# Performance work log

Measured on AMD Instinct MI355X. Metric: run time of the kernel, lower is better.

## Reference

```python
import jax, jax.numpy as jnp
import numpy as np

N_NODES = 50000
N_EDGES = 800000
EMB = 96
HID = 2 * EMB


def setup_inputs() -> dict:
    key = jax.random.key(0)
    ks = jax.random.split(key, 8)
    h = jax.random.normal(ks[0], (N_NODES, EMB), dtype=jnp.float32)
    edge_attr = jax.random.normal(ks[1], (N_EDGES, EMB), dtype=jnp.float32)
    src = jax.random.randint(ks[2], (N_EDGES,), 0, N_NODES, dtype=jnp.int32)
    dst = jax.random.randint(ks[3], (N_EDGES,), 0, N_NODES, dtype=jnp.int32)
    W1 = jax.random.normal(ks[4], (EMB, HID), dtype=jnp.float32) * (1.0 / np.sqrt(EMB))
    b1 = jnp.zeros((HID,), dtype=jnp.float32)
    W2 = jax.random.normal(ks[5], (HID, EMB), dtype=jnp.float32) * (1.0 / np.sqrt(HID))
    b2 = jnp.zeros((EMB,), dtype=jnp.float32)
    eps = jnp.zeros((1,), dtype=jnp.float32)
    return {"h": h, "edge_attr": edge_attr, "src": src, "dst": dst,
            "W1": W1, "b1": b1, "W2": W2, "b2": b2, "eps": eps}


def reference(h, edge_attr, src, dst, W1, b1, W2, b2, eps):
    # message: m_e = h[src_e] + edge_attr_e   -> [E, EMB]
    m = h[src] + edge_attr
    # reduce: sum messages per destination node -> [N, EMB]
    aggr = jax.ops.segment_sum(m, dst, num_segments=N_NODES)
    # 2-layer MLP: Linear(EMB, 2*EMB) -> ReLU -> Linear(2*EMB, EMB)
    hidden = jax.nn.relu(aggr @ W1 + b1)
    mlp_out = hidden @ W2 + b2
    # GIN update: (1 + eps) * h + MLP(aggr)
    out = (1.0 + eps[0]) * h + mlp_out
    return out
```

## Files before the change

### kernel.cpp

```cpp
#include <hip/hip_runtime.h>

#define N_NODES 50000
#define N_EDGES 800000
#define EMB 96
#define HID 192

#define HIST_BLOCKS ((N_EDGES + 255) / 256)
#define CONV_BLOCKS ((2 * EMB * HID + 255) / 256)

typedef __attribute__((ext_vector_type(8))) short short8;
typedef __attribute__((ext_vector_type(4))) float f32x4;
typedef __attribute__((ext_vector_type(4))) unsigned short ushort4v;

static __device__ __forceinline__ unsigned short f2bf(float f) {
    union { float f; unsigned int u; } v; v.f = f;
    unsigned int u = v.u;
    return (unsigned short)((u + 0x7FFFu + ((u >> 16) & 1u)) >> 16);
}

__global__ __launch_bounds__(256) void hist_conv_kernel(
    const int* __restrict__ dst, int* __restrict__ counts,
    const float* __restrict__ W1, const float* __restrict__ W2,
    unsigned short* __restrict__ W1t, unsigned short* __restrict__ W2t)
{
    int b = blockIdx.x;
    if (b < HIST_BLOCKS) {
        int e = b * 256 + threadIdx.x;
        if (e < N_EDGES) atomicAdd(&counts[dst[e]], 1);
    } else {
        int i = (b - HIST_BLOCKS) * 256 + threadIdx.x;
        if (i < EMB * HID) {
            int n = i / EMB, k = i % EMB;
            W1t[i] = f2bf(W1[(size_t)k * HID + n]);
        } else if (i < 2 * EMB * HID) {
            int j = i - EMB * HID;
            int n = j / HID, k = j % HID;
            W2t[j] = f2bf(W2[(size_t)k * EMB + n]);
        }
    }
}

__global__ __launch_bounds__(1024) void scan_kernel(
    const int* __restrict__ counts, int* __restrict__ offsets)
{
    __shared__ int wave_sums[16];
    int t = threadIdx.x;
    int lane = t & 63, wave = t >> 6;
    int running = 0;
    int v_next = (t < N_NODES) ? counts[t] : 0;
    for (int base = 0; base < N_NODES; base += 1024) {
        int v = v_next;
        int nidx = base + 1024 + t;
        v_next = (nidx < N_NODES) ? counts[nidx] : 0;
        int x = v;
        #pragma unroll
        for (int d = 1; d < 64; d <<= 1) {
            int y = __shfl_up(x, d);
            if (lane >= d) x += y;
        }
        if (lane == 63) wave_sums[wave] = x;
        __syncthreads();
        if (t < 16) {
            int s = wave_sums[t];
            #pragma unroll
            for (int d = 1; d < 16; d <<= 1) {
                int y = __shfl_up(s, d);
                if (t >= d) s += y;
            }
            wave_sums[t] = s;
        }
        __syncthreads();
        int woff = wave ? wave_sums[wave - 1] : 0;
        if (base + t < N_NODES) offsets[base + t] = running + woff + x - v;
        int total = wave_sums[15];
        __syncthreads();
        running += total;
    }
    if (t == 0) offsets[N_NODES] = running;
}

__global__ __launch_bounds__(256) void fill_kernel(
    const int* __restrict__ src, const int* __restrict__ dst,
    const int* __restrict__ offsets, int* __restrict__ cursor,
    int2* __restrict__ pairs)
{
    int e = blockIdx.x * 256 + threadIdx.x;
    if (e < N_EDGES) {
        int d = dst[e];
        int pos = offsets[d] + atomicAdd(&cursor[d], 1);
        pairs[pos] = make_int2(e, src[e]);
    }
}

__global__ __launch_bounds__(192) void gather_kernel4(
    const f32x4* __restrict__ h4, const f32x4* __restrict__ ea4,
    const int* __restrict__ offsets, const int2* __restrict__ pairs,
    unsigned short* __restrict__ aggr_bf)
{
    int n = blockIdx.x * 8 + threadIdx.x / 24;
    int c = threadIdx.x % 24;
    if (n >= N_NODES) return;
    int beg = offsets[n], end = offsets[n + 1];
    f32x4 a0 = {0.f, 0.f, 0.f, 0.f}, a1 = a0, a2 = a0, a3 = a0;
    int i = beg;
    for (; i + 4 <= end; i += 4) {
        int2 q0 = pairs[i], q1 = pairs[i + 1], q2 = pairs[i + 2], q3 = pairs[i + 3];
        f32x4 e0 = __builtin_nontemporal_load(&ea4[(size_t)q0.x * 24 + c]);
        f32x4 e1 = __builtin_nontemporal_load(&ea4[(size_t)q1.x * 24 + c]);
        f32x4 e2 = __builtin_nontemporal_load(&ea4[(size_t)q2.x * 24 + c]);
        f32x4 e3 = __builtin_nontemporal_load(&ea4[(size_t)q3.x * 24 + c]);
        f32x4 g0 = h4[(size_t)q0.y * 24 + c];
        f32x4 g1 = h4[(size_t)q1.y * 24 + c];
        f32x4 g2 = h4[(size_t)q2.y * 24 + c];
        f32x4 g3 = h4[(size_t)q3.y * 24 + c];
        a0 += e0 + g0;
        a1 += e1 + g1;
        a2 += e2 + g2;
        a3 += e3 + g3;
    }
    for (; i < end; ++i) {
        int2 q = pairs[i];
        f32x4 e = __builtin_nontemporal_load(&ea4[(size_t)q.x * 24 + c]);
        f32x4 g = h4[(size_t)q.y * 24 + c];
        a0 += e + g;
    }
    f32x4 acc = (a0 + a1) + (a2 + a3);
    ushort4v o;
    o.x = f2bf(acc.x); o.y = f2bf(acc.y); o.z = f2bf(acc.z); o.w = f2bf(acc.w);
    *(ushort4v*)(aggr_bf + (size_t)n * EMB + c * 4) = o;
}

__global__ __launch_bounds__(256) void mlp_fused(
    const unsigned short* __restrict__ aggr_bf,
    const unsigned short* __restrict__ W1t, const float* __restrict__ b1,
    const unsigned short* __restrict__ W2t, const float* __restrict__ b2,
    const float* __restrict__ h, const float* __restrict__ eps,
    float* __restrict__ out)
{
    __shared__ unsigned short sW1[HID * 104];
    int t = threadIdx.x;
    const unsigned int* p1 = (const unsigned int*)W1t;
    for (int i = t; i < HID * (EMB / 2); i += 256) {
        int n = i / (EMB / 2), c2 = i % (EMB / 2);
        *(unsigned int*)&sW1[n * 104 + c2 * 2] = p1[(size_t)n * (EMB / 2) + c2];
    }
    __syncthreads();

    int wave = t >> 6, lane = t & 63;
    int m0 = (blockIdx.x * 4 + wave) * 16;
    bool active = (m0 < N_NODES);
    int quad = lane >> 4, col = lane & 15;
    int m = m0 + col;

    f32x4 acc1[12];
    #pragma unroll
    for (int c = 0; c < 12; ++c) acc1[c] = (f32x4){0.f, 0.f, 0.f, 0.f};
    if (active) {
        #pragma unroll
        for (int ks = 0; ks < 3; ++ks) {
            short8 af = *(const short8*)(aggr_bf + (size_t)m * EMB + ks * 32 + quad * 8);
            #pragma unroll
            for (int c = 0; c < 12; ++c) {
                short8 bf = *(const short8*)(sW1 + (c * 16 + col) * 104 + ks * 32 + quad * 8);
                acc1[c] = __builtin_amdgcn_mfma_f32_16x16x32_bf16(af, bf, acc1[c], 0, 0, 0);
            }
        }
    }
    __syncthreads();

    if (active) {
        unsigned short* sH = sW1 + wave * (16 * 200);
        #pragma unroll
        for (int c = 0; c < 12; ++c) {
            float bias = b1[c * 16 + col];
            #pragma unroll
            for (int r = 0; r < 4; ++r) {
                int lr = quad * 4 + r;
                sH[lr * 200 + c * 16 + col] = f2bf(fmaxf(acc1[c][r] + bias, 0.f));
            }
        }
        f32x4 acc2[6];
        #pragma unroll
        for (int c = 0; c < 6; ++c) acc2[c] = (f32x4){0.f, 0.f, 0.f, 0.f};
        #pragma unroll
        for (int ks = 0; ks < 6; ++ks) {
            short8 af = *(const short8*)(sH + col * 200 + ks * 32 + quad * 8);
            #pragma unroll
            for (int c = 0; c < 6; ++c) {
                short8 bf = *(const short8*)(W2t + (size_t)(c * 16 + col) * HID + ks * 32 + quad * 8);
                acc2[c] = __builtin_amdgcn_mfma_f32_16x16x32_bf16(af, bf, acc2[c], 0, 0, 0);
            }
        }
        float s = 1.f + eps[0];
        #pragma unroll
        for (int c = 0; c < 6; ++c) {
            float bias = b2[c * 16 + col];
            #pragma unroll
            for (int r = 0; r < 4; ++r) {
                int row = m0 + quad * 4 + r;
                size_t idx = (size_t)row * EMB + c * 16 + col;
                out[idx] = acc2[c][r] + bias + s * h[idx];
            }
        }
    }
}

extern "C" void kernel_launch(void* const* d_in, const int* in_sizes, int n_in,
                              void* d_out, int out_size, void* d_ws, size_t ws_size,
                              hipStream_t stream) {
    const float* h         = (const float*)d_in[0];
    const float* edge_attr = (const float*)d_in[1];
    const int*   src       = (const int*)d_in[2];
    const int*   dst       = (const int*)d_in[3];
    const float* W1        = (const float*)d_in[4];
    const float* b1        = (const float*)d_in[5];
    const float* W2        = (const float*)d_in[6];
    const float* b2        = (const float*)d_in[7];
    const float* eps       = (const float*)d_in[8];
    float* out = (float*)d_out;

    unsigned char* wsp = (unsigned char*)d_ws;
    unsigned short* aggr_bf = (unsigned short*)wsp; wsp += (size_t)N_NODES * EMB * 2;
    unsigned short* W1t     = (unsigned short*)wsp; wsp += (size_t)EMB * HID * 2;
    unsigned short* W2t     = (unsigned short*)wsp; wsp += (size_t)EMB * HID * 2;
    int2* pairs   = (int2*)wsp; wsp += (size_t)N_EDGES * sizeof(int2);
    int*  offsets = (int*)wsp;  wsp += (size_t)(N_NODES + 1) * sizeof(int);
    int*  counts  = (int*)wsp;  wsp += (size_t)N_NODES * sizeof(int);
    int*  cursor  = (int*)wsp;

    hipMemsetAsync(counts, 0, (size_t)2 * N_NODES * sizeof(int), stream);

    hist_conv_kernel<<<HIST_BLOCKS + CONV_BLOCKS, 256, 0, stream>>>(
        dst, counts, W1, W2, W1t, W2t);
    scan_kernel<<<1, 1024, 0, stream>>>(counts, offsets);
    fill_kernel<<<(N_EDGES + 255) / 256, 256, 0, stream>>>(src, dst, offsets, cursor, pairs);
    gather_kernel4<<<(N_NODES + 7) / 8, 192, 0, stream>>>(
        (const f32x4*)h, (const f32x4*)edge_attr, offsets, pairs, aggr_bf);
    mlp_fused<<<(N_NODES / 16 + 3) / 4, 256, 0, stream>>>(
        aggr_bf, W1t, b1, W2t, b2, h, eps, out);
}
```

Before: 596.7 us.

## Fuse all stages into one persistent kernel with software grid barriers

Replaces the five separate launches (histogram/convert, scan, fill, gather, MLP) with a single persistent kernel of 512 blocks that loops over work and synchronises stages with an atomic grid barrier. The single-block serial scan becomes a two-level parallel scan over per-block sums. This removes launch gaps and the serial scan, but relies on all 512 blocks being co-resident. It also cuts gather and MLP parallelism to a fixed grid, and the gather uses 32-thread groups with 8 of them idle.

```diff
diff --git a/kernel.cpp b/kernel.cpp
--- a/kernel.cpp
+++ b/kernel.cpp
@@ -5,8 +5,9 @@
 #define EMB 96
 #define HID 192
 
-#define HIST_BLOCKS ((N_EDGES + 255) / 256)
-#define CONV_BLOCKS ((2 * EMB * HID + 255) / 256)
+#define NB 512
+#define NT 256
+#define GSIZE (NB * NT)
 
 typedef __attribute__((ext_vector_type(8))) short short8;
 typedef __attribute__((ext_vector_type(4))) float f32x4;
@@ -18,188 +19,198 @@
     return (unsigned short)((u + 0x7FFFu + ((u >> 16) & 1u)) >> 16);
 }
 
-__global__ __launch_bounds__(256) void hist_conv_kernel(
-    const int* __restrict__ dst, int* __restrict__ counts,
-    const float* __restrict__ W1, const float* __restrict__ W2,
-    unsigned short* __restrict__ W1t, unsigned short* __restrict__ W2t)
+struct Params {
+    const float* h; const float* ea; const int* src; const int* dst;
+    const float* W1; const float* b1; const float* W2; const float* b2;
+    const float* eps; float* out;
+    unsigned short* aggr_bf; unsigned short* W1t; unsigned short* W2t;
+    int2* pairs; int* offsets; int* counts; int* cursor;
+    int* bar;
+    int* bsum; int* bpref;
+};
+
+static __device__ __forceinline__ void grid_barrier(int* arrive, int* gen) {
+    __syncthreads();
+    if (threadIdx.x == 0) {
+        int g = __hip_atomic_load(gen, __ATOMIC_RELAXED, __HIP_MEMORY_SCOPE_AGENT);
+        __threadfence();
+        int prev = __hip_atomic_fetch_add(arrive, 1, __ATOMIC_ACQ_REL,
+                                          __HIP_MEMORY_SCOPE_AGENT);
+        if (prev == NB - 1) {
+            __hip_atomic_store(arrive, 0, __ATOMIC_RELAXED, __HIP_MEMORY_SCOPE_AGENT);
+            __hip_atomic_fetch_add(gen, 1, __ATOMIC_RELEASE, __HIP_MEMORY_SCOPE_AGENT);
+        } else {
+            while (__hip_atomic_load(gen, __ATOMIC_ACQUIRE,
+                                     __HIP_MEMORY_SCOPE_AGENT) == g)
+                __builtin_amdgcn_s_sleep(1);
+        }
+    }
+    __syncthreads();
+    __threadfence();
+}
+
+__global__ __launch_bounds__(NT, 2) void mega_kernel(Params p)
 {
-    int b = blockIdx.x;
-    if (b < HIST_BLOCKS) {
-        int e = b * 256 + threadIdx.x;
-        if (e < N_EDGES) atomicAdd(&counts[dst[e]], 1);
-    } else {
-        int i = (b - HIST_BLOCKS) * 256 + threadIdx.x;
-        if (i < EMB * HID) {
-            int n = i / EMB, k = i % EMB;
-            W1t[i] = f2bf(W1[(size_t)k * HID + n]);
-        } else if (i < 2 * EMB * HID) {
-            int j = i - EMB * HID;
-            int n = j / HID, k = j % HID;
-            W2t[j] = f2bf(W2[(size_t)k * EMB + n]);
-        }
-    }
-}
-
-__global__ __launch_bounds__(1024) void scan_kernel(
-    const int* __restrict__ counts, int* __restrict__ offsets)
-{
-    __shared__ int wave_sums[16];
-    int t = threadIdx.x;
-    int lane = t & 63, wave = t >> 6;
-    int running = 0;
-    int v_next = (t < N_NODES) ? counts[t] : 0;
-    for (int base = 0; base < N_NODES; base += 1024) {
-        int v = v_next;
-        int nidx = base + 1024 + t;
-        v_next = (nidx < N_NODES) ? counts[nidx] : 0;
-        int x = v;
+    __shared__ __attribute__((aligned(16))) unsigned char smem[65536];
+    const int t = threadIdx.x, b = blockIdx.x;
+    const int gid = b * NT + t;
+    const int lane = t & 63, wave = t >> 6;
+
+    for (int e = gid; e < N_EDGES; e += GSIZE)
+        atomicAdd(&p.counts[p.dst[e]], 1);
+    for (int i = gid; i < EMB * HID; i += GSIZE) {
+        int n = i / EMB, k = i - n * EMB;
+        p.W1t[i] = f2bf(p.W1[(size_t)k * HID + n]);
+    }
+    for (int i = gid; i < EMB * HID; i += GSIZE) {
+        int n = i / HID, k = i - n * HID;
+        p.W2t[i] = f2bf(p.W2[(size_t)k * EMB + n]);
+    }
+    grid_barrier(&p.bar[0], &p.bar[1]);
+
+    int* ws4 = (int*)smem;
+    int v = (gid < N_NODES) ? p.counts[gid] : 0;
+    int x = v;
+    #pragma unroll
+    for (int d = 1; d < 64; d <<= 1) { int y = __shfl_up(x, d); if (lane >= d) x += y; }
+    if (lane == 63) ws4[wave] = x;
+    __syncthreads();
+    int s0 = ws4[0], s1 = ws4[1], s2 = ws4[2], s3 = ws4[3];
+    int wbase = (wave > 0 ? s0 : 0) + (wave > 1 ? s1 : 0) + (wave > 2 ? s2 : 0);
+    int locex = wbase + x - v;
+    if (t == 0) p.bsum[b] = s0 + s1 + s2 + s3;
+    grid_barrier(&p.bar[0], &p.bar[1]);
+
+    if (b == 0) {
+        int carry = 0;
         #pragma unroll
-        for (int d = 1; d < 64; d <<= 1) {
-            int y = __shfl_up(x, d);
-            if (lane >= d) x += y;
-        }
-        if (lane == 63) wave_sums[wave] = x;
+        for (int half = 0; half < NB / NT; ++half) {
+            int a = p.bsum[half * NT + t];
+            int xx = a;
+            #pragma unroll
+            for (int d = 1; d < 64; d <<= 1) { int y = __shfl_up(xx, d); if (lane >= d) xx += y; }
+            if (lane == 63) ws4[wave] = xx;
+            __syncthreads();
+            int q0 = ws4[0], q1 = ws4[1], q2 = ws4[2], q3 = ws4[3];
+            int wb = (wave > 0 ? q0 : 0) + (wave > 1 ? q1 : 0) + (wave > 2 ? q2 : 0);
+            p.bpref[half * NT + t] = carry + wb + xx - a;
+            __syncthreads();
+            carry += q0 + q1 + q2 + q3;
+        }
+    }
+    grid_barrier(&p.bar[0], &p.bar[1]);
+
+    if (gid < N_NODES) p.offsets[gid] = p.bpref[b] + locex;
+    if (gid == 0) p.offsets[N_NODES] = N_EDGES;
+    grid_barrier(&p.bar[0], &p.bar[1]);
+
+    for (int e = gid; e < N_EDGES; e += GSIZE) {
+        int d = p.dst[e];
+        int pos = p.offsets[d] + atomicAdd(&p.cursor[d], 1);
+        p.pairs[pos] = make_int2(e, p.src[e]);
+    }
+    grid_barrier(&p.bar[0], &p.bar[1]);
+
+    {
+        const f32x4* h4 = (const f32x4*)p.h;
+        const f32x4* ea4 = (const f32x4*)p.ea;
+        int g = t >> 5, c = t & 31;
+        for (int n = b * 8 + g; n < N_NODES; n += NB * 8) {
+            int beg = p.offsets[n], end = p.offsets[n + 1];
+            if (c < 24) {
+                f32x4 a0 = {0.f, 0.f, 0.f, 0.f}, a1 = a0, a2 = a0, a3 = a0;
+                int i = beg;
+                for (; i + 4 <= end; i += 4) {
+                    int2 q0 = p.pairs[i], q1 = p.pairs[i + 1];
+                    int2 q2 = p.pairs[i + 2], q3 = p.pairs[i + 3];
+                    f32x4 e0 = __builtin_nontemporal_load(&ea4[(size_t)q0.x * 24 + c]);
+                    f32x4 e1 = __builtin_nontemporal_load(&ea4[(size_t)q1.x * 24 + c]);
+                    f32x4 e2 = __builtin_nontemporal_load(&ea4[(size_t)q2.x * 24 + c]);
+                    f32x4 e3 = __builtin_nontemporal_load(&ea4[(size_t)q3.x * 24 + c]);
+                    f32x4 g0 = h4[(size_t)q0.y * 24 + c];
+                    f32x4 g1 = h4[(size_t)q1.y * 24 + c];
+                    f32x4 g2 = h4[(size_t)q2.y * 24 + c];
+                    f32x4 g3 = h4[(size_t)q3.y * 24 + c];
+                    a0 += e0 + g0;
+                    a1 += e1 + g1;
+                    a2 += e2 + g2;
+                    a3 += e3 + g3;
+                }
+                for (; i < end; ++i) {
+                    int2 q = p.pairs[i];
+                    f32x4 e = __builtin_nontemporal_load(&ea4[(size_t)q.x * 24 + c]);
+                    f32x4 gg = h4[(size_t)q.y * 24 + c];
+                    a0 += e + gg;
+                }
+                f32x4 acc = (a0 + a1) + (a2 + a3);
+                ushort4v o;
+                o.x = f2bf(acc.x); o.y = f2bf(acc.y);
+                o.z = f2bf(acc.z); o.w = f2bf(acc.w);
+                *(ushort4v*)(p.aggr_bf + (size_t)n * EMB + c * 4) = o;
+            }
+        }
+    }
+    grid_barrier(&p.bar[0], &p.bar[1]);
+
+    {
+        unsigned short* sW1 = (unsigned short*)smem;
+        unsigned short* sHid = (unsigned short*)(smem + HID * 104 * 2);
+        const unsigned int* p1 = (const unsigned int*)p.W1t;
+        for (int i = t; i < HID * (EMB / 2); i += NT) {
+            int n = i / (EMB / 2), c2 = i - n * (EMB / 2);
+            *(unsigned int*)&sW1[n * 104 + c2 * 2] = p1[n * (EMB / 2) + c2];
+        }
         __syncthreads();
-        if (t < 16) {
-            int s = wave_sums[t];
-            #pragma unroll
-            for (int d = 1; d < 16; d <<= 1) {
-                int y = __shfl_up(s, d);
-                if (t >= d) s += y;
-            }
-            wave_sums[t] = s;
-        }
-        __syncthreads();
-        int woff = wave ? wave_sums[wave - 1] : 0;
-        if (base + t < N_NODES) offsets[base + t] = running + woff + x - v;
-        int total = wave_sums[15];
-        __syncthreads();
-        running += total;
-    }
-    if (t == 0) offsets[N_NODES] = running;
-}
-
-__global__ __launch_bounds__(256) void fill_kernel(
-    const int* __restrict__ src, const int* __restrict__ dst,
-    const int* __restrict__ offsets, int* __restrict__ cursor,
-    int2* __restrict__ pairs)
-{
-    int e = blockIdx.x * 256 + threadIdx.x;
-    if (e < N_EDGES) {
-        int d = dst[e];
-        int pos = offsets[d] + atomicAdd(&cursor[d], 1);
-        pairs[pos] = make_int2(e, src[e]);
-    }
-}
-
-__global__ __launch_bounds__(192) void gather_kernel4(
-    const f32x4* __restrict__ h4, const f32x4* __restrict__ ea4,
-    const int* __restrict__ offsets, const int2* __restrict__ pairs,
-    unsigned short* __restrict__ aggr_bf)
-{
-    int n = blockIdx.x * 8 + threadIdx.x / 24;
-    int c = threadIdx.x % 24;
-    if (n >= N_NODES) return;
-    int beg = offsets[n], end = offsets[n + 1];
-    f32x4 a0 = {0.f, 0.f, 0.f, 0.f}, a1 = a0, a2 = a0, a3 = a0;
-    int i = beg;
-    for (; i + 4 <= end; i += 4) {
-        int2 q0 = pairs[i], q1 = pairs[i + 1], q2 = pairs[i + 2], q3 = pairs[i + 3];
-        f32x4 e0 = __builtin_nontemporal_load(&ea4[(size_t)q0.x * 24 + c]);
-        f32x4 e1 = __builtin_nontemporal_load(&ea4[(size_t)q1.x * 24 + c]);
-        f32x4 e2 = __builtin_nontemporal_load(&ea4[(size_t)q2.x * 24 + c]);
-        f32x4 e3 = __builtin_nontemporal_load(&ea4[(size_t)q3.x * 24 + c]);
-        f32x4 g0 = h4[(size_t)q0.y * 24 + c];
-        f32x4 g1 = h4[(size_t)q1.y * 24 + c];
-        f32x4 g2 = h4[(size_t)q2.y * 24 + c];
-        f32x4 g3 = h4[(size_t)q3.y * 24 + c];
-        a0 += e0 + g0;
-        a1 += e1 + g1;
-        a2 += e2 + g2;
-        a3 += e3 + g3;
-    }
-    for (; i < end; ++i) {
-        int2 q = pairs[i];
-        f32x4 e = __builtin_nontemporal_load(&ea4[(size_t)q.x * 24 + c]);
-        f32x4 g = h4[(size_t)q.y * 24 + c];
-        a0 += e + g;
-    }
-    f32x4 acc = (a0 + a1) + (a2 + a3);
-    ushort4v o;
-    o.x = f2bf(acc.x); o.y = f2bf(acc.y); o.z = f2bf(acc.z); o.w = f2bf(acc.w);
-    *(ushort4v*)(aggr_bf + (size_t)n * EMB + c * 4) = o;
-}
-
-__global__ __launch_bounds__(256) void mlp_fused(
-    const unsigned short* __restrict__ aggr_bf,
-    const unsigned short* __restrict__ W1t, const float* __restrict__ b1,
-    const unsigned short* __restrict__ W2t, const float* __restrict__ b2,
-    const float* __restrict__ h, const float* __restrict__ eps,
-    float* __restrict__ out)
-{
-    __shared__ unsigned short sW1[HID * 104];
-    int t = threadIdx.x;
-    const unsigned int* p1 = (const unsigned int*)W1t;
-    for (int i = t; i < HID * (EMB / 2); i += 256) {
-        int n = i / (EMB / 2), c2 = i % (EMB / 2);
-        *(unsigned int*)&sW1[n * 104 + c2 * 2] = p1[(size_t)n * (EMB / 2) + c2];
-    }
-    __syncthreads();
-
-    int wave = t >> 6, lane = t & 63;
-    int m0 = (blockIdx.x * 4 + wave) * 16;
-    bool active = (m0 < N_NODES);
-    int quad = lane >> 4, col = lane & 15;
-    int m = m0 + col;
-
-    f32x4 acc1[12];
-    #pragma unroll
-    for (int c = 0; c < 12; ++c) acc1[c] = (f32x4){0.f, 0.f, 0.f, 0.f};
-    if (active) {
-        #pragma unroll
-        for (int ks = 0; ks < 3; ++ks) {
-            short8 af = *(const short8*)(aggr_bf + (size_t)m * EMB + ks * 32 + quad * 8);
+        int quad = lane >> 4, col = lane & 15;
+        float s = 1.f + p.eps[0];
+        unsigned short* sH = sHid + wave * (16 * 200);
+        for (int rb = b; rb < (N_NODES + 63) / 64; rb += NB) {
+            int m0 = rb * 64 + wave * 16;
+            if (m0 >= N_NODES) continue;
+            int m = m0 + col;
+
+            f32x4 acc1[12];
+            #pragma unroll
+            for (int c = 0; c < 12; ++c) acc1[c] = (f32x4){0.f, 0.f, 0.f, 0.f};
+            #pragma unroll
+            for (int ks = 0; ks < 3; ++ks) {
+                short8 af = *(const short8*)(p.aggr_bf + (size_t)m * EMB + ks * 32 + quad * 8);
+                #pragma unroll
+                for (int c = 0; c < 12; ++c) {
+                    short8 bf = *(const short8*)(sW1 + (c * 16 + col) * 104 + ks * 32 + quad * 8);
+                    acc1[c] = __builtin_amdgcn_mfma_f32_16x16x32_bf16(af, bf, acc1[c], 0, 0, 0);
+                }
+            }
             #pragma unroll
             for (int c = 0; c < 12; ++c) {
-                short8 bf = *(const short8*)(sW1 + (c * 16 + col) * 104 + ks * 32 + quad * 8);
-                acc1[c] = __builtin_amdgcn_mfma_f32_16x16x32_bf16(af, bf, acc1[c], 0, 0, 0);
-            }
-        }
-    }
-    __syncthreads();
-
-    if (active) {
-        unsigned short* sH = sW1 + wave * (16 * 200);
-        #pragma unroll
-        for (int c = 0; c < 12; ++c) {
-            float bias = b1[c * 16 + col];
-            #pragma unroll
-            for (int r = 0; r < 4; ++r) {
-                int lr = quad * 4 + r;
-                sH[lr * 200 + c * 16 + col] = f2bf(fmaxf(acc1[c][r] + bias, 0.f));
-            }
-        }
-        f32x4 acc2[6];
-        #pragma unroll
-        for (int c = 0; c < 6; ++c) acc2[c] = (f32x4){0.f, 0.f, 0.f, 0.f};
-        #pragma unroll
-        for (int ks = 0; ks < 6; ++ks) {
-            short8 af = *(const short8*)(sH + col * 200 + ks * 32 + quad * 8);
+                float bias = p.b1[c * 16 + col];
+                #pragma unroll
+                for (int r = 0; r < 4; ++r) {
+                    int lr = quad * 4 + r;
+                    sH[lr * 200 + c * 16 + col] = f2bf(fmaxf(acc1[c][r] + bias, 0.f));
+                }
+            }
+            f32x4 acc2[6];
+            #pragma unroll
+            for (int c = 0; c < 6; ++c) acc2[c] = (f32x4){0.f, 0.f, 0.f, 0.f};
+            #pragma unroll
+            for (int ks = 0; ks < 6; ++ks) {
+                short8 af = *(const short8*)(sH + col * 200 + ks * 32 + quad * 8);
+                #pragma unroll
+                for (int c = 0; c < 6; ++c) {
+                    short8 bf = *(const short8*)(p.W2t + (size_t)(c * 16 + col) * HID + ks * 32 + quad * 8);
+                    acc2[c] = __builtin_amdgcn_mfma_f32_16x16x32_bf16(af, bf, acc2[c], 0, 0, 0);
+                }
+            }
             #pragma unroll
             for (int c = 0; c < 6; ++c) {
-                short8 bf = *(const short8*)(W2t + (size_t)(c * 16 + col) * HID + ks * 32 + quad * 8);
-                acc2[c] = __builtin_amdgcn_mfma_f32_16x16x32_bf16(af, bf, acc2[c], 0, 0, 0);
-            }
-        }
-        float s = 1.f + eps[0];
-        #pragma unroll
-        for (int c = 0; c < 6; ++c) {
-            float bias = b2[c * 16 + col];
-            #pragma unroll
-            for (int r = 0; r < 4; ++r) {
-                int row = m0 + quad * 4 + r;
-                size_t idx = (size_t)row * EMB + c * 16 + col;
-                out[idx] = acc2[c][r] + bias + s * h[idx];
+                float bias = p.b2[c * 16 + col];
+                #pragma unroll
+                for (int r = 0; r < 4; ++r) {
+                    int row = m0 + quad * 4 + r;
+                    size_t idx = (size_t)row * EMB + c * 16 + col;
+                    p.out[idx] = acc2[c][r] + bias + s * p.h[idx];
+                }
             }
         }
     }
@@ -208,34 +219,31 @@
 extern "C" void kernel_launch(void* const* d_in, const int* in_sizes, int n_in,
                               void* d_out, int out_size, void* d_ws, size_t ws_size,
                               hipStream_t stream) {
-    const float* h         = (const float*)d_in[0];
-    const float* edge_attr = (const float*)d_in[1];
-    const int*   src       = (const int*)d_in[2];
-    const int*   dst       = (const int*)d_in[3];
-    const float* W1        = (const float*)d_in[4];
-    const float* b1        = (const float*)d_in[5];
-    const float* W2        = (const float*)d_in[6];
-    const float* b2        = (const float*)d_in[7];
-    const float* eps       = (const float*)d_in[8];
-    float* out = (float*)d_out;
+    Params p;
+    p.h   = (const float*)d_in[0];
+    p.ea  = (const float*)d_in[1];
+    p.src = (const int*)d_in[2];
+    p.dst = (const int*)d_in[3];
+    p.W1  = (const float*)d_in[4];
+    p.b1  = (const float*)d_in[5];
+    p.W2  = (const float*)d_in[6];
+    p.b2  = (const float*)d_in[7];
+    p.eps = (const float*)d_in[8];
+    p.out = (float*)d_out;
 
     unsigned char* wsp = (unsigned char*)d_ws;
-    unsigned short* aggr_bf = (unsigned short*)wsp; wsp += (size_t)N_NODES * EMB * 2;
-    unsigned short* W1t     = (unsigned short*)wsp; wsp += (size_t)EMB * HID * 2;
-    unsigned short* W2t     = (unsigned short*)wsp; wsp += (size_t)EMB * HID * 2;
-    int2* pairs   = (int2*)wsp; wsp += (size_t)N_EDGES * sizeof(int2);
-    int*  offsets = (int*)wsp;  wsp += (size_t)(N_NODES + 1) * sizeof(int);
-    int*  counts  = (int*)wsp;  wsp += (size_t)N_NODES * sizeof(int);
-    int*  cursor  = (int*)wsp;
-
-    hipMemsetAsync(counts, 0, (size_t)2 * N_NODES * sizeof(int), stream);
-
-    hist_conv_kernel<<<HIST_BLOCKS + CONV_BLOCKS, 256, 0, stream>>>(
-        dst, counts, W1, W2, W1t, W2t);
-    scan_kernel<<<1, 1024, 0, stream>>>(counts, offsets);
-    fill_kernel<<<(N_EDGES + 255) / 256, 256, 0, stream>>>(src, dst, offsets, cursor, pairs);
-    gather_kernel4<<<(N_NODES + 7) / 8, 192, 0, stream>>>(
-        (const f32x4*)h, (const f32x4*)edge_attr, offsets, pairs, aggr_bf);
-    mlp_fused<<<(N_NODES / 16 + 3) / 4, 256, 0, stream>>>(
-        aggr_bf, W1t, b1, W2t, b2, h, eps, out);
-}
+    p.aggr_bf = (unsigned short*)wsp; wsp += (size_t)N_NODES * EMB * 2;
+    p.W1t     = (unsigned short*)wsp; wsp += (size_t)EMB * HID * 2;
+    p.W2t     = (unsigned short*)wsp; wsp += (size_t)EMB * HID * 2;
+    p.pairs   = (int2*)wsp; wsp += (size_t)N_EDGES * sizeof(int2);
+    p.offsets = (int*)wsp;  wsp += (size_t)(N_NODES + 1) * sizeof(int);
+    p.counts  = (int*)wsp;  wsp += (size_t)N_NODES * sizeof(int);
+    p.cursor  = (int*)wsp;  wsp += (size_t)N_NODES * sizeof(int);
+    p.bar     = (int*)wsp;  wsp += 2 * sizeof(int);
+    p.bsum    = (int*)wsp;  wsp += (size_t)NB * sizeof(int);
+    p.bpref   = (int*)wsp;
+
+    hipMemsetAsync(p.counts, 0, ((size_t)2 * N_NODES + 2) * sizeof(int), stream);
+
+    hipLaunchKernelGGL(mega_kernel, dim3(NB), dim3(NT), 0, stream, p);
+}
```

Result: slower. 1.161 ms (+94.5%).
